# Optimization experiments

Measured on AMD Instinct MI355X. Metric: run time of the kernel, lower is better.

Reference implementation:

```python
import jax, jax.numpy as jnp
import numpy as np

DIM = 4096
N_HEADS = 32
N_KV_HEADS = 8
HEAD_DIM = DIM // N_HEADS  # 128
N_REP = N_HEADS // N_KV_HEADS  # 4
BSZ = 2
SEQ = 2048
ROPE_THETA = 500000.0


def setup_inputs() -> dict:
    key = jax.random.key(0)
    ks = jax.random.split(key, 10)
    x = jax.random.normal(ks[0], (BSZ, SEQ, DIM), dtype=jnp.float32)
    # RoPE frequencies (Llama style): theta^{-2i/d}, angles = pos * freq
    inv_freq = 1.0 / (ROPE_THETA ** (jnp.arange(0, HEAD_DIM, 2, dtype=jnp.float32) / HEAD_DIM))  # [64]
    angles = jnp.arange(SEQ, dtype=jnp.float32)[:, None] * inv_freq[None, :]  # [SEQ, 64]
    freqs_cos = jnp.cos(angles)
    freqs_sin = jnp.sin(angles)
    # causal additive mask for prefill
    mask = jnp.triu(jnp.full((SEQ, SEQ), -jnp.inf, dtype=jnp.float32), k=1)
    scale = 0.02
    wq = jax.random.normal(ks[1], (DIM, DIM), dtype=jnp.float32) * scale
    bq = jnp.zeros((DIM,), dtype=jnp.float32)
    wk = jax.random.normal(ks[2], (N_KV_HEADS * HEAD_DIM, DIM), dtype=jnp.float32) * scale
    bk = jnp.zeros((N_KV_HEADS * HEAD_DIM,), dtype=jnp.float32)
    wv = jax.random.normal(ks[3], (N_KV_HEADS * HEAD_DIM, DIM), dtype=jnp.float32) * scale
    bv = jnp.zeros((N_KV_HEADS * HEAD_DIM,), dtype=jnp.float32)
    wo = jax.random.normal(ks[4], (DIM, DIM), dtype=jnp.float32) * scale
    bo = jnp.zeros((DIM,), dtype=jnp.float32)
    return {"x": x, "freqs_cos": freqs_cos, "freqs_sin": freqs_sin, "mask": mask,
            "wq": wq, "bq": bq, "wk": wk, "bk": bk, "wv": wv, "bv": bv, "wo": wo, "bo": bo}


def _apply_rope(t, cos, sin):
    # t: [b, s, h, d]; cos/sin: [s, d//2]; pairs are consecutive (view_as_complex)
    a = t[..., 0::2]
    b = t[..., 1::2]
    cos = cos[None, :, None, :]
    sin = sin[None, :, None, :]
    out_a = a * cos - b * sin
    out_b = a * sin + b * cos
    return jnp.stack([out_a, out_b], axis=-1).reshape(t.shape)


def reference(x, freqs_cos, freqs_sin, mask, wq, bq, wk, bk, wv, bv, wo, bo):
    bsz, seq_len, _ = x.shape
    xq = (x @ wq.T + bq).reshape(bsz, seq_len, N_HEADS, HEAD_DIM)
    xk = (x @ wk.T + bk).reshape(bsz, seq_len, N_KV_HEADS, HEAD_DIM)
    xv = (x @ wv.T + bv).reshape(bsz, seq_len, N_KV_HEADS, HEAD_DIM)
    xq = _apply_rope(xq, freqs_cos, freqs_sin)
    xk = _apply_rope(xk, freqs_cos, freqs_sin)
    # start_pos=0 prefill: cache write then slice [:, :seq_len] returns xk/xv
    keys, values = xk, xv
    # repeat_kv via GQA grouping inside einsum (equivalent to materialized expand)
    # q: [b, s, kvh, rep, d]
    q = xq.reshape(bsz, seq_len, N_KV_HEADS, N_REP, HEAD_DIM)
    scores = jnp.einsum('bqgrd,bkgd->bgrqk', q, keys) / jnp.sqrt(jnp.float32(HEAD_DIM))
    scores = scores + mask[None, None, None, :, :]
    probs = jax.nn.softmax(scores.astype(jnp.float32), axis=-1).astype(xq.dtype)
    out = jnp.einsum('bgrqk,bkgd->bqgrd', probs, values)
    out = out.reshape(bsz, seq_len, DIM)
    return out @ wo.T + bo
```

## Files before the change

### kernel.cpp

```cpp
#include <hip/hip_runtime.h>


using bf16x8 = __attribute__((ext_vector_type(8))) short;
using f32x4  = __attribute__((ext_vector_type(4))) float;
using u16x4  = __attribute__((ext_vector_type(4))) unsigned short;
using u16x8  = __attribute__((ext_vector_type(8))) unsigned short;

__device__ __forceinline__ float bf2f(unsigned short h) {
    unsigned int u = ((unsigned int)h) << 16;
    return __builtin_bit_cast(float, u);
}
__device__ __forceinline__ unsigned short f2bf(float f) {
    unsigned int u = __builtin_bit_cast(unsigned int, f);
    u += 0x7FFFu + ((u >> 16) & 1u);
    return (unsigned short)(u >> 16);
}
__device__ __forceinline__ f32x4 mfma16(bf16x8 a, bf16x8 b, f32x4 c) {
    return __builtin_amdgcn_mfma_f32_16x16x32_bf16(a, b, c, 0, 0, 0);
}

#define GLOAD_LDS16(gp, lp)                                                   \
    __builtin_amdgcn_global_load_lds(                                         \
        (const __attribute__((address_space(1))) void*)(gp),                  \
        (__attribute__((address_space(3))) void*)(lp), 16, 0, 0)

__global__ __launch_bounds__(256) void cvt_kernel(
    const float* __restrict__ src, unsigned short* __restrict__ dst, int n)
{
    const int i = (blockIdx.x * 256 + threadIdx.x) * 8;
    if (i >= n) return;
    float4 a = *(const float4*)(src + i);
    float4 b = *(const float4*)(src + i + 4);
    u16x8 o;
    o[0] = f2bf(a.x); o[1] = f2bf(a.y); o[2] = f2bf(a.z); o[3] = f2bf(a.w);
    o[4] = f2bf(b.x); o[5] = f2bf(b.y); o[6] = f2bf(b.z); o[7] = f2bf(b.w);
    *(u16x8*)(dst + i) = o;
}

template<int MODE>
__global__ __launch_bounds__(512, 2) void gemm256(
    const unsigned short* __restrict__ A, const unsigned short* __restrict__ W,
    const float* __restrict__ bias, void* __restrict__ Cv,
    int M, int N, int K)
{
    __shared__ __align__(16) unsigned short As[3][256 * 32];
    __shared__ __align__(16) unsigned short Bs[3][256 * 32];

    const int nwg  = gridDim.x * gridDim.y;
    const int bid0 = blockIdx.y * gridDim.x + blockIdx.x;
    const int bid  = (bid0 & 7) * (nwg >> 3) + (bid0 >> 3);
    const int bx = bid % gridDim.x, by = bid / gridDim.x;

    const int tid  = threadIdx.x;
    const int lane = tid & 63;
    const int wid  = tid >> 6;
    const int ln = lane & 15, quad = lane >> 4;
    const int wr = wid >> 2, wc = wid & 3;
    const int m0 = by * 256, n0 = bx * 256;

    const int srow  = tid >> 2;
    const int sgran = (tid & 3) ^ ((tid >> 3) & 3);
    const unsigned short* aptr = A + (size_t)(m0 + srow) * K + sgran * 8;
    const unsigned short* bptr = W + (size_t)(n0 + srow) * K + sgran * 8;
    const size_t rowskip = (size_t)128 * K;

#define G256_STAGE(ab, bb)                                                    \
    do {                                                                      \
        GLOAD_LDS16(aptr,           (ab) + tid * 8);                          \
        GLOAD_LDS16(aptr + rowskip, (ab) + 4096 + tid * 8);                   \
        GLOAD_LDS16(bptr,           (bb) + tid * 8);                          \
        GLOAD_LDS16(bptr + rowskip, (bb) + 4096 + tid * 8);                   \
        aptr += 32; bptr += 32;                                               \
    } while (0)

    f32x4 acc[8][4];
#pragma unroll
    for (int i = 0; i < 8; ++i)
#pragma unroll
        for (int j = 0; j < 4; ++j) acc[i][j] = f32x4{0.f, 0.f, 0.f, 0.f};

    unsigned short *a0 = As[0], *a1 = As[1], *a2 = As[2];
    unsigned short *b0 = Bs[0], *b1 = Bs[1], *b2 = Bs[2];

    const int nk = K >> 5;
    G256_STAGE(a0, b0);
    G256_STAGE(a1, b1);
    asm volatile("s_waitcnt vmcnt(4)" ::: "memory");
    __builtin_amdgcn_s_barrier();

    const int swz  = (quad ^ ((ln >> 1) & 3)) * 8;
    const int aoff = (wr * 128 + ln) * 32 + swz;
    const int boff = (wc * 64 + ln) * 32 + swz;

    for (int kt = 0; kt < nk; ++kt) {
        const bool more = (kt + 2 < nk);
        if (more) G256_STAGE(a2, b2);

        bf16x8 af[8], bfr[4];
#pragma unroll
        for (int i = 0; i < 8; ++i) af[i]  = *(const bf16x8*)(a0 + aoff + i * 512);
#pragma unroll
        for (int j = 0; j < 4; ++j) bfr[j] = *(const bf16x8*)(b0 + boff + j * 512);

        __builtin_amdgcn_s_setprio(1);
#pragma unroll
        for (int i = 0; i < 8; ++i)
#pragma unroll
            for (int j = 0; j < 4; ++j)
                acc[i][j] = mfma16(af[i], bfr[j], acc[i][j]);
        __builtin_amdgcn_s_setprio(0);

        if (more) asm volatile("s_waitcnt vmcnt(4) lgkmcnt(0)" ::: "memory");
        else      asm volatile("s_waitcnt vmcnt(0) lgkmcnt(0)" ::: "memory");
        __builtin_amdgcn_s_barrier();

        unsigned short* t;
        t = a0; a0 = a1; a1 = a2; a2 = t;
        t = b0; b0 = b1; b1 = b2; b2 = t;
    }
#undef G256_STAGE

#pragma unroll
    for (int j = 0; j < 4; ++j) {
        const int col = n0 + wc * 64 + j * 16 + ln;
        const float bval = bias[col];
#pragma unroll
        for (int i = 0; i < 8; ++i) {
            const int rowb = m0 + wr * 128 + i * 16 + quad * 4;
            if (MODE == 2) {
                float* C = (float*)Cv;
#pragma unroll
                for (int r = 0; r < 4; ++r)
                    C[(size_t)(rowb + r) * N + col] = acc[i][j][r] + bval;
            } else {
                unsigned short* C = (unsigned short*)Cv;
#pragma unroll
                for (int r = 0; r < 4; ++r)
                    C[(size_t)(rowb + r) * N + col] = f2bf(acc[i][j][r] + bval);
            }
        }
    }
}

template<int MODE>
__global__ __launch_bounds__(256) void gemm_bias(
    const unsigned short* __restrict__ A, const unsigned short* __restrict__ W,
    const float* __restrict__ bias, const float* __restrict__ bias2,
    void* __restrict__ Cv, void* __restrict__ Cv2,
    int M, int N, int K)
{
    __shared__ __align__(16) unsigned short As[2][128 * 32];
    __shared__ __align__(16) unsigned short Bs[2][128 * 32];

    const int tid  = threadIdx.x;
    const int lane = tid & 63;
    const int wv   = tid >> 6;
    const int ln   = lane & 15, quad = lane >> 4;
    const int wr   = wv >> 1, wc = wv & 1;
    const int m0 = blockIdx.y * 128 + wr * 64;
    const int n0 = blockIdx.x * 128 + wc * 64;

    const int srow  = tid >> 2;
    const int sgran = (tid & 3) ^ ((tid >> 3) & 3);
    const unsigned short* aptr = A + (size_t)(blockIdx.y * 128 + srow) * K + sgran * 8;
    const unsigned short* bptr = W + (size_t)(blockIdx.x * 128 + srow) * K + sgran * 8;
    const size_t rowskip = (size_t)64 * K;

#define GEMM_STAGE(c)                                                         \
    do {                                                                      \
        GLOAD_LDS16(aptr,           &As[c][tid * 8]);                         \
        GLOAD_LDS16(aptr + rowskip, &As[c][2048 + tid * 8]);                  \
        GLOAD_LDS16(bptr,           &Bs[c][tid * 8]);                         \
        GLOAD_LDS16(bptr + rowskip, &Bs[c][2048 + tid * 8]);                  \
        aptr += 32; bptr += 32;                                               \
    } while (0)

    f32x4 acc[4][4];
#pragma unroll
    for (int i = 0; i < 4; ++i)
#pragma unroll
        for (int j = 0; j < 4; ++j) acc[i][j] = f32x4{0.f, 0.f, 0.f, 0.f};

    GEMM_STAGE(0);
    __syncthreads();

    const int swz = (quad ^ ((ln >> 1) & 3)) * 8;

    const int nk = K >> 5;
    int cur = 0;
    for (int kt = 0; kt < nk; ++kt) {
        if (kt + 1 < nk) GEMM_STAGE(cur ^ 1);

        bf16x8 af[4], bfr[4];
#pragma unroll
        for (int i = 0; i < 4; ++i)
            af[i]  = *(const bf16x8*)(&As[cur][(wr * 64 + i * 16 + ln) * 32 + swz]);
#pragma unroll
        for (int j = 0; j < 4; ++j)
            bfr[j] = *(const bf16x8*)(&Bs[cur][(wc * 64 + j * 16 + ln) * 32 + swz]);
#pragma unroll
        for (int i = 0; i < 4; ++i)
#pragma unroll
            for (int j = 0; j < 4; ++j)
                acc[i][j] = mfma16(af[i], bfr[j], acc[i][j]);

        __syncthreads();
        cur ^= 1;
    }
#undef GEMM_STAGE

#pragma unroll
    for (int j = 0; j < 4; ++j) {
        const int col = n0 + j * 16 + ln;
        const float bval = (MODE == 1 && col >= 1024) ? bias2[col - 1024] : bias[col];
#pragma unroll
        for (int i = 0; i < 4; ++i) {
            const int rowb = m0 + i * 16 + quad * 4;
            if (MODE == 0) {
                unsigned short* C = (unsigned short*)Cv;
#pragma unroll
                for (int r = 0; r < 4; ++r)
                    C[(size_t)(rowb + r) * N + col] = f2bf(acc[i][j][r] + bval);
            } else {
                if (col < 1024) {
                    unsigned short* C = (unsigned short*)Cv;
#pragma unroll
                    for (int r = 0; r < 4; ++r)
                        C[(size_t)(rowb + r) * 1024 + col] = f2bf(acc[i][j][r] + bval);
                } else {
                    unsigned short* C = (unsigned short*)Cv2;
                    const int vcol = col - 1024;
                    const int gg = vcol >> 7, d = vcol & 127;
                    const int bb = rowb >> 11, s = rowb & 2047;
                    u16x4 pk;
#pragma unroll
                    for (int r = 0; r < 4; ++r) pk[r] = f2bf(acc[i][j][r] + bval);
                    *(u16x4*)(C + (((size_t)(bb * 8 + gg) * 128 + d) * 2048 + s)) = pk;
                }
            }
        }
    }
}

__global__ __launch_bounds__(256) void rope_kernel(
    unsigned short* __restrict__ Q, unsigned short* __restrict__ Kb,
    const float* __restrict__ fc, const float* __restrict__ fs)
{
    const int idx = blockIdx.x * 256 + threadIdx.x;
    const int NQP = 2 * 2048 * 32 * 64;
    const int NKP = 2 * 2048 * 8 * 64;
    unsigned short* t; int s, i; float scale;
    if (idx < NQP) {
        i = idx & 63; const int bsh = idx >> 6;
        s = (bsh >> 5) & 2047;
        t = Q + ((size_t)bsh << 7) + 2 * i;
        scale = 0.12751743f;
    } else {
        const int p = idx - NQP;
        if (p >= NKP) return;
        i = p & 63; const int bsh = p >> 6;
        s = (bsh >> 3) & 2047;
        t = Kb + ((size_t)bsh << 7) + 2 * i;
        scale = 1.0f;
    }
    const float c = fc[s * 64 + i], sn = fs[s * 64 + i];
    const unsigned int u = *(const unsigned int*)t;
    const float a = bf2f((unsigned short)(u & 0xffff));
    const float b = bf2f((unsigned short)(u >> 16));
    const unsigned int lo = f2bf((a * c - b * sn) * scale);
    const unsigned int hi = f2bf((a * sn + b * c) * scale);
    *(unsigned int*)t = lo | (hi << 16);
}

__global__ __launch_bounds__(512, 4) void attn_kernel(
    const unsigned short* __restrict__ Q, const unsigned short* __restrict__ K,
    const unsigned short* __restrict__ Vt, unsigned short* __restrict__ O)
{
    __shared__ __align__(16) unsigned short Ks[2][32 * 128];
    __shared__ __align__(16) unsigned short Vs[2][128 * 32];
    __shared__ __align__(16) unsigned short p_s[8][16][40];

    const int tid  = threadIdx.x;
    const int lane = tid & 63;
    const int wv   = tid >> 6;
    const int ln = lane & 15, quad = lane >> 4;
    const int bx = blockIdx.x;
    const int g = bx & 7, b = (bx >> 3) & 1;
    const int pairIdx = bx >> 4;
    const int h = wv >> 1;
    const int rh = (wv & 1) * 16;

    const int krow = tid >> 4, kcs = (tid & 15) ^ (krow & 7);
    const int vrow = tid >> 2, vcs = (tid & 3) ^ (vrow & 3);
    const unsigned short* ksrc0 =
        K + ((size_t)(b * 2048 + krow) * 8 + g) * 128 + kcs * 8;
    const unsigned short* vsrc0 =
        Vt + (size_t)(b * 8 + g) * 262144 + (size_t)vrow * 2048 + vcs * 8;

#define ATTN_STAGE(c)                                                         \
    do {                                                                      \
        GLOAD_LDS16(ksrc, &Ks[c][tid * 8]);                                   \
        GLOAD_LDS16(vsrc, &Vs[c][tid * 8]);                                   \
        ksrc += 32768; vsrc += 32;                                            \
    } while (0)

#pragma unroll
    for (int ph = 0; ph < 2; ++ph) {
        const int j   = ph ? (63 - pairIdx) : pairIdx;
        const int q0w = j * 32 + rh;
        const int nk  = j + 1;

        bf16x8 qf[4];
        {
            const unsigned short* qrow =
                Q + ((size_t)((b * 2048 + q0w + ln) * 32 + g * 4 + h)) * 128 + quad * 8;
#pragma unroll
            for (int d4 = 0; d4 < 4; ++d4) qf[d4] = *(const bf16x8*)(qrow + d4 * 32);
        }

        f32x4 oacc[8];
#pragma unroll
        for (int t = 0; t < 8; ++t) oacc[t] = f32x4{0.f, 0.f, 0.f, 0.f};
        float li[4] = {0.f, 0.f, 0.f, 0.f};

        const unsigned short* ksrc = ksrc0;
        const unsigned short* vsrc = vsrc0;

        ATTN_STAGE(0);
        __syncthreads();

        for (int kt = 0; kt < nk; ++kt) {
            const int cur = kt & 1;
            const int k0  = kt * 32;
            if (kt + 1 < nk) ATTN_STAGE(cur ^ 1);

            const bool edge = (kt == nk - 1);
            const unsigned short* Kc = Ks[cur];
            const unsigned short* Vc = Vs[cur];

            bf16x8 kf0[4], kf1[4];
#pragma unroll
            for (int d4 = 0; d4 < 4; ++d4) {
                const int isw = ((d4 * 4 + quad) ^ (ln & 7)) * 8;
                kf0[d4] = *(const bf16x8*)(Kc + ln * 128 + isw);
                kf1[d4] = *(const bf16x8*)(Kc + (16 + ln) * 128 + isw);
            }
            f32x4 s0 = f32x4{0.f, 0.f, 0.f, 0.f};
            f32x4 s1 = f32x4{0.f, 0.f, 0.f, 0.f};
#pragma unroll
            for (int d4 = 0; d4 < 4; ++d4) s0 = mfma16(qf[d4], kf0[d4], s0);
#pragma unroll
            for (int d4 = 0; d4 < 4; ++d4) s1 = mfma16(qf[d4], kf1[d4], s1);
#pragma unroll
            for (int r = 0; r < 4; ++r) {
                float e0 = __builtin_amdgcn_exp2f(s0[r]);
                float e1 = __builtin_amdgcn_exp2f(s1[r]);
                if (edge) {
                    const int qg = q0w + quad * 4 + r;
                    e0 = (k0 + ln <= qg)      ? e0 : 0.f;
                    e1 = (k0 + 16 + ln <= qg) ? e1 : 0.f;
                }
                li[r] += e0 + e1;
                p_s[wv][quad * 4 + r][ln]      = f2bf(e0);
                p_s[wv][quad * 4 + r][16 + ln] = f2bf(e1);
            }
            __asm__ volatile("s_waitcnt lgkmcnt(0)" ::: "memory");
            bf16x8 pf = *(const bf16x8*)(&p_s[wv][ln][quad * 8]);
            const int vsw = (quad ^ (ln & 3)) * 8;
#pragma unroll
            for (int t = 0; t < 8; ++t) {
                bf16x8 vf = *(const bf16x8*)(Vc + (t * 16 + ln) * 32 + vsw);
                oacc[t] = mfma16(pf, vf, oacc[t]);
            }
            __syncthreads();
        }

        float inv[4];
#pragma unroll
        for (int r = 0; r < 4; ++r) {
            float l = li[r];
#pragma unroll
            for (int off = 1; off < 16; off <<= 1) l += __shfl_xor(l, off);
            inv[r] = 1.0f / l;
        }
        unsigned short* ob =
            O + ((size_t)((b * 2048 + q0w + quad * 4) * 32 + g * 4 + h)) * 128;
#pragma unroll
        for (int t = 0; t < 8; ++t)
#pragma unroll
            for (int r = 0; r < 4; ++r)
                ob[(size_t)r * 4096 + t * 16 + ln] = f2bf(oacc[t][r] * inv[r]);
    }
#undef ATTN_STAGE
}

extern "C" void kernel_launch(void* const* d_in, const int* in_sizes, int n_in,
                              void* d_out, int out_size, void* d_ws, size_t ws_size,
                              hipStream_t stream)
{
    const float* x  = (const float*)d_in[0];
    const float* fc = (const float*)d_in[1];
    const float* fs = (const float*)d_in[2];
    const float* wq = (const float*)d_in[4];
    const float* bq = (const float*)d_in[5];
    const float* wk = (const float*)d_in[6];
    const float* bk = (const float*)d_in[7];
    const float* wv = (const float*)d_in[8];
    const float* bv = (const float*)d_in[9];
    const float* wo = (const float*)d_in[10];
    const float* bo = (const float*)d_in[11];

    unsigned short* wsp = (unsigned short*)d_ws;
    unsigned short* xb  = wsp;
    unsigned short* wqb = xb  + 16777216;
    unsigned short* wkb = wqb + 16777216;
    unsigned short* wvb = wkb + 4194304;
    unsigned short* Qb  = wvb + 4194304;
    unsigned short* Kb  = Qb  + 16777216;
    unsigned short* Vt  = Kb  + 4194304;

    cvt_kernel<<<8192, 256, 0, stream>>>(x,  xb,  16777216);
    cvt_kernel<<<8192, 256, 0, stream>>>(wq, wqb, 16777216);
    cvt_kernel<<<2048, 256, 0, stream>>>(wk, wkb, 4194304);
    cvt_kernel<<<2048, 256, 0, stream>>>(wv, wvb, 4194304);

    gemm256<0><<<dim3(16, 16), 512, 0, stream>>>(xb, wqb, bq, Qb, 4096, 4096, 4096);
    gemm_bias<1><<<dim3(16, 32), 256, 0, stream>>>(xb, wkb, bk, bv,
                                                   Kb, Vt, 4096, 2048, 4096);

    cvt_kernel<<<8192, 256, 0, stream>>>(wo, wqb, 16777216);

    rope_kernel<<<40960, 256, 0, stream>>>(Qb, Kb, fc, fs);
    attn_kernel<<<512, 512, 0, stream>>>(Qb, Kb, Vt, xb);

    gemm256<2><<<dim3(16, 16), 512, 0, stream>>>(xb, wqb, bo,
                                                 d_out, 4096, 4096, 4096);
}
```

Baseline: 768.4 us.

## Deepen LDS prefetch pipelines in both bf16 GEMM kernels

The 256-tile GEMM moves from a three-stage to a four-stage global-to-LDS ring buffer, so three tiles are in flight, with vmcnt waits tuned to the remaining iterations. The 128-tile GEMM moves from double buffering with __syncthreads to a three-stage rotating buffer with explicit vmcnt waits and MFMA priority boosting. The aim is to hide global-load latency behind matrix-core work. The cost is more LDS per block, which may limit blocks per CU.

```diff
diff --git a/kernel.cpp b/kernel.cpp
--- a/kernel.cpp
+++ b/kernel.cpp
@@ -43,8 +43,8 @@
     const float* __restrict__ bias, void* __restrict__ Cv,
     int M, int N, int K)
 {
-    __shared__ __align__(16) unsigned short As[3][256 * 32];
-    __shared__ __align__(16) unsigned short Bs[3][256 * 32];
+    __shared__ __align__(16) unsigned short As[4][256 * 32];
+    __shared__ __align__(16) unsigned short Bs[4][256 * 32];
 
     const int nwg  = gridDim.x * gridDim.y;
     const int bid0 = blockIdx.y * gridDim.x + blockIdx.x;
@@ -79,13 +79,14 @@
 #pragma unroll
         for (int j = 0; j < 4; ++j) acc[i][j] = f32x4{0.f, 0.f, 0.f, 0.f};
 
-    unsigned short *a0 = As[0], *a1 = As[1], *a2 = As[2];
-    unsigned short *b0 = Bs[0], *b1 = Bs[1], *b2 = Bs[2];
+    unsigned short *a0 = As[0], *a1 = As[1], *a2 = As[2], *a3 = As[3];
+    unsigned short *b0 = Bs[0], *b1 = Bs[1], *b2 = Bs[2], *b3 = Bs[3];
 
     const int nk = K >> 5;
     G256_STAGE(a0, b0);
     G256_STAGE(a1, b1);
-    asm volatile("s_waitcnt vmcnt(4)" ::: "memory");
+    G256_STAGE(a2, b2);
+    asm volatile("s_waitcnt vmcnt(8)" ::: "memory");
     __builtin_amdgcn_s_barrier();
 
     const int swz  = (quad ^ ((ln >> 1) & 3)) * 8;
@@ -93,8 +94,7 @@
     const int boff = (wc * 64 + ln) * 32 + swz;
 
     for (int kt = 0; kt < nk; ++kt) {
-        const bool more = (kt + 2 < nk);
-        if (more) G256_STAGE(a2, b2);
+        if (kt + 3 < nk) G256_STAGE(a3, b3);
 
         bf16x8 af[8], bfr[4];
 #pragma unroll
@@ -110,13 +110,15 @@
                 acc[i][j] = mfma16(af[i], bfr[j], acc[i][j]);
         __builtin_amdgcn_s_setprio(0);
 
-        if (more) asm volatile("s_waitcnt vmcnt(4) lgkmcnt(0)" ::: "memory");
-        else      asm volatile("s_waitcnt vmcnt(0) lgkmcnt(0)" ::: "memory");
+        const int rem = nk - 1 - kt;
+        if (rem >= 3)      asm volatile("s_waitcnt vmcnt(8) lgkmcnt(0)" ::: "memory");
+        else if (rem == 2) asm volatile("s_waitcnt vmcnt(4) lgkmcnt(0)" ::: "memory");
+        else               asm volatile("s_waitcnt vmcnt(0) lgkmcnt(0)" ::: "memory");
         __builtin_amdgcn_s_barrier();
 
         unsigned short* t;
-        t = a0; a0 = a1; a1 = a2; a2 = t;
-        t = b0; b0 = b1; b1 = b2; b2 = t;
+        t = a0; a0 = a1; a1 = a2; a2 = a3; a3 = t;
+        t = b0; b0 = b1; b1 = b2; b2 = b3; b3 = t;
     }
 #undef G256_STAGE
 
@@ -149,8 +151,8 @@
     void* __restrict__ Cv, void* __restrict__ Cv2,
     int M, int N, int K)
 {
-    __shared__ __align__(16) unsigned short As[2][128 * 32];
-    __shared__ __align__(16) unsigned short Bs[2][128 * 32];
+    __shared__ __align__(16) unsigned short As[3][128 * 32];
+    __shared__ __align__(16) unsigned short Bs[3][128 * 32];
 
     const int tid  = threadIdx.x;
     const int lane = tid & 63;
@@ -166,12 +168,12 @@
     const unsigned short* bptr = W + (size_t)(blockIdx.x * 128 + srow) * K + sgran * 8;
     const size_t rowskip = (size_t)64 * K;
 
-#define GEMM_STAGE(c)                                                         \
+#define GEMM_STAGE(ab, bb)                                                    \
     do {                                                                      \
-        GLOAD_LDS16(aptr,           &As[c][tid * 8]);                         \
-        GLOAD_LDS16(aptr + rowskip, &As[c][2048 + tid * 8]);                  \
-        GLOAD_LDS16(bptr,           &Bs[c][tid * 8]);                         \
-        GLOAD_LDS16(bptr + rowskip, &Bs[c][2048 + tid * 8]);                  \
+        GLOAD_LDS16(aptr,           (ab) + tid * 8);                          \
+        GLOAD_LDS16(aptr + rowskip, (ab) + 2048 + tid * 8);                   \
+        GLOAD_LDS16(bptr,           (bb) + tid * 8);                          \
+        GLOAD_LDS16(bptr + rowskip, (bb) + 2048 + tid * 8);                   \
         aptr += 32; bptr += 32;                                               \
     } while (0)
 
@@ -181,31 +183,44 @@
 #pragma unroll
         for (int j = 0; j < 4; ++j) acc[i][j] = f32x4{0.f, 0.f, 0.f, 0.f};
 
-    GEMM_STAGE(0);
-    __syncthreads();
+    unsigned short *a0 = As[0], *a1 = As[1], *a2 = As[2];
+    unsigned short *b0 = Bs[0], *b1 = Bs[1], *b2 = Bs[2];
+
+    const int nk = K >> 5;
+    GEMM_STAGE(a0, b0);
+    GEMM_STAGE(a1, b1);
+    asm volatile("s_waitcnt vmcnt(4)" ::: "memory");
+    __builtin_amdgcn_s_barrier();
 
     const int swz = (quad ^ ((ln >> 1) & 3)) * 8;
 
-    const int nk = K >> 5;
-    int cur = 0;
     for (int kt = 0; kt < nk; ++kt) {
-        if (kt + 1 < nk) GEMM_STAGE(cur ^ 1);
+        if (kt + 2 < nk) GEMM_STAGE(a2, b2);
 
         bf16x8 af[4], bfr[4];
 #pragma unroll
         for (int i = 0; i < 4; ++i)
-            af[i]  = *(const bf16x8*)(&As[cur][(wr * 64 + i * 16 + ln) * 32 + swz]);
+            af[i]  = *(const bf16x8*)(a0 + (wr * 64 + i * 16 + ln) * 32 + swz);
 #pragma unroll
         for (int j = 0; j < 4; ++j)
-            bfr[j] = *(const bf16x8*)(&Bs[cur][(wc * 64 + j * 16 + ln) * 32 + swz]);
+            bfr[j] = *(const bf16x8*)(b0 + (wc * 64 + j * 16 + ln) * 32 + swz);
+
+        __builtin_amdgcn_s_setprio(1);
 #pragma unroll
         for (int i = 0; i < 4; ++i)
 #pragma unroll
             for (int j = 0; j < 4; ++j)
                 acc[i][j] = mfma16(af[i], bfr[j], acc[i][j]);
-
-        __syncthreads();
-        cur ^= 1;
+        __builtin_amdgcn_s_setprio(0);
+
+        const int rem = nk - 1 - kt;
+        if (rem >= 2) asm volatile("s_waitcnt vmcnt(4) lgkmcnt(0)" ::: "memory");
+        else          asm volatile("s_waitcnt vmcnt(0) lgkmcnt(0)" ::: "memory");
+        __builtin_amdgcn_s_barrier();
+
+        unsigned short* t;
+        t = a0; a0 = a1; a1 = a2; a2 = t;
+        t = b0; b0 = b1; b1 = b2; b2 = t;
     }
 #undef GEMM_STAGE
 
```

New measurement: 779.7 us. No clear change (+1.5%).
